# Kernel optimization log

Measured on AMD Instinct MI355X. Metric: run time of the kernel, lower is better.

## Reference

```python
import jax, jax.numpy as jnp
import numpy as np

B, R, C, NH = 8, 64, 256, 8
N = R * R            # 4096 tokens
HD = C // NH         # head dim 32
FF = 3               # focusing factor

def dwconv(x, w, b):
    # x: (B, C, H, W); w: (C, 1, kh, kw) depthwise
    y = jax.lax.conv_general_dilated(
        x, w, window_strides=(1, 1), padding='SAME',
        dimension_numbers=('NCHW', 'OIHW', 'NCHW'),
        feature_group_count=x.shape[1])
    return y + b[None, :, None, None]

def setup_inputs() -> dict:
    key = jax.random.key(0)
    ks = jax.random.split(key, 6)
    return {
        'qkv': jax.random.normal(ks[0], (3, B, N, C), jnp.float32),
        'pos_enc': jax.random.normal(ks[1], (1, N, C), jnp.float32) * 0.02,
        'scale': jax.random.normal(ks[2], (1, 1, C), jnp.float32) * 0.02,
        'w_v': jax.random.normal(ks[3], (C, 1, 3, 3), jnp.float32) * 0.1,
        'b_v': jnp.zeros((C,), jnp.float32),
        'w_dwc': jax.random.normal(ks[4], (HD, 1, 5, 5), jnp.float32) * 0.1,
        'b_dwc': jnp.zeros((HD,), jnp.float32),
    }

def reference(qkv, pos_enc, scale, w_v, b_v, w_dwc, b_dwc):
    q, k, v = qkv[0], qkv[1], qkv[2]          # each (B, N, C)
    # --- LePE: depthwise 3x3 conv on v over full channel dim ---
    v_img = v.transpose(0, 2, 1).reshape(B, C, R, R)
    lepe = dwconv(v_img, w_v, b_v)            # (B, C, R, R)
    lepe = lepe.reshape(B * NH, HD, N).transpose(0, 2, 1)   # (B*h, N, hd)
    v = v_img.reshape(B, C, N).transpose(0, 2, 1)           # (B, N, C)
    # --- focused kernelization ---
    k = k + pos_enc
    sc = jax.nn.softplus(scale)
    q = (jax.nn.relu(q) + 1e-6) / sc
    k = (jax.nn.relu(k) + 1e-6) / sc
    qn = jnp.linalg.norm(q, axis=-1, keepdims=True)
    kn = jnp.linalg.norm(k, axis=-1, keepdims=True)
    q = q ** FF
    k = k ** FF
    q = q / jnp.linalg.norm(q, axis=-1, keepdims=True) * qn
    k = k / jnp.linalg.norm(k, axis=-1, keepdims=True) * kn
    split = lambda x: x.reshape(B, N, NH, HD).transpose(0, 2, 1, 3).reshape(B * NH, N, HD)
    q, k, v = split(q), split(k), split(v)    # (B*h, N, hd)
    # --- linear attention (kv aggregation path: N >> hd) ---
    z = 1.0 / (jnp.einsum('bic,bc->bi', q, k.sum(axis=1)) + 1e-6)
    kv = jnp.einsum('bjc,bjd->bcd', k, v)     # (B*h, hd, hd)
    x = jnp.einsum('bic,bcd,bi->bid', q, kv, z)
    # --- dwc feature mixing on v per head ---
    fm = v.transpose(0, 2, 1).reshape(B * NH, HD, R, R)
    fm = dwconv(fm, w_dwc, b_dwc).reshape(B * NH, HD, N).transpose(0, 2, 1)
    x = x + fm + lepe
    x = x.reshape(B, NH, N, HD).transpose(0, 2, 1, 3).reshape(B, N, C)
    return x
```

## Files before the change

### kernel.cpp

```cpp
#include <hip/hip_runtime.h>
#include <math.h>

#define B_  8
#define R_  64
#define C_  256
#define NH_ 8
#define N_  4096
#define HD_ 32

__device__ __forceinline__ float softplus_rcp(float s) {
    return 1.f / __logf(1.f + __expf(s));
}

__global__ __launch_bounds__(256) void kernelNB2(
        const float* __restrict__ qkv, const float* __restrict__ pos,
        const float* __restrict__ scale,
        float* __restrict__ qs_arr, float* __restrict__ part,
        float* __restrict__ kspart) {
    __shared__ float smem[9472];
    float* kf_s   = smem;
    float* v_s    = smem + 4096;
    float* rsc_s  = smem + 8192;
    float* kred_s = smem + 8448;

    const int t    = threadIdx.x;
    const int wave = t >> 6, lane = t & 63;
    const int c0   = lane * 4;
    const int blk  = blockIdx.x;
    const int tok0 = blk * 32;

    if (t < C_) rsc_s[t] = softplus_rcp(scale[t]);
    __syncthreads();

    const size_t qbase = (size_t)tok0 * C_;
    const size_t kbase = (size_t)B_ * N_ * C_ + qbase;
    const size_t vbase = (size_t)2 * B_ * N_ * C_ + qbase;

    const int h  = t >> 5;
    const int l  = t & 31;
    const int cg = l & 7;
    const int dg = l >> 3;

    const float rs0 = rsc_s[c0 + 0], rs1 = rsc_s[c0 + 1];
    const float rs2 = rsc_s[c0 + 2], rs3 = rsc_s[c0 + 3];

    float acc[4][8];
    #pragma unroll
    for (int ii = 0; ii < 4; ii++)
        #pragma unroll
        for (int jj = 0; jj < 8; jj++) acc[ii][jj] = 0.f;
    float ksp[4] = {0.f, 0.f, 0.f, 0.f};

    for (int tile = 0; tile < 2; tile++) {
        const int nb0 = tile * 16;
        #pragma unroll
        for (int i = 0; i < 4; i++) {
            const int row = wave * 4 + i;
            const int tok = tok0 + nb0 + row;
            const int n   = tok & (N_ - 1);
            const size_t off = (size_t)(nb0 + row) * C_ + c0;
            const float4 q4 = *(const float4*)(qkv + qbase + off);
            const float4 k4 = *(const float4*)(qkv + kbase + off);
            const float4 v4 = *(const float4*)(qkv + vbase + off);
            const float4 p4 = *(const float4*)(pos + (size_t)n * C_ + c0);

            const float qv0 = (fmaxf(q4.x, 0.f) + 1e-6f) * rs0;
            const float qv1 = (fmaxf(q4.y, 0.f) + 1e-6f) * rs1;
            const float qv2 = (fmaxf(q4.z, 0.f) + 1e-6f) * rs2;
            const float qv3 = (fmaxf(q4.w, 0.f) + 1e-6f) * rs3;
            const float kw0 = (fmaxf(k4.x + p4.x, 0.f) + 1e-6f) * rs0;
            const float kw1 = (fmaxf(k4.y + p4.y, 0.f) + 1e-6f) * rs1;
            const float kw2 = (fmaxf(k4.z + p4.z, 0.f) + 1e-6f) * rs2;
            const float kw3 = (fmaxf(k4.w + p4.w, 0.f) + 1e-6f) * rs3;

            const float q30 = qv0 * qv0 * qv0, q31 = qv1 * qv1 * qv1;
            const float q32 = qv2 * qv2 * qv2, q33 = qv3 * qv3 * qv3;
            const float k30 = kw0 * kw0 * kw0, k31 = kw1 * kw1 * kw1;
            const float k32 = kw2 * kw2 * kw2, k33 = kw3 * kw3 * kw3;

            float sq2 = qv0 * qv0 + qv1 * qv1 + qv2 * qv2 + qv3 * qv3;
            float sq6 = q30 * q30 + q31 * q31 + q32 * q32 + q33 * q33;
            float sk2 = kw0 * kw0 + kw1 * kw1 + kw2 * kw2 + kw3 * kw3;
            float sk6 = k30 * k30 + k31 * k31 + k32 * k32 + k33 * k33;
            #pragma unroll
            for (int m = 1; m < 64; m <<= 1) {
                sq2 += __shfl_xor(sq2, m, 64);
                sq6 += __shfl_xor(sq6, m, 64);
                sk2 += __shfl_xor(sk2, m, 64);
                sk6 += __shfl_xor(sk6, m, 64);
            }
            if (lane == 0) qs_arr[tok] = sqrtf(sq2) * rsqrtf(sq6);
            const float ks = sqrtf(sk2) * rsqrtf(sk6);

            float4 kf;
            kf.x = k30 * ks;  kf.y = k31 * ks;
            kf.z = k32 * ks;  kf.w = k33 * ks;
            *(float4*)&kf_s[row * C_ + c0] = kf;
            *(float4*)&v_s [row * C_ + c0] = v4;
            ksp[0] += kf.x;  ksp[1] += kf.y;
            ksp[2] += kf.z;  ksp[3] += kf.w;
        }
        __syncthreads();
        {
            const float* kfp = kf_s + h * HD_ + cg * 4;
            const float* vp  = v_s  + h * HD_ + dg * 8;
            #pragma unroll 4
            for (int nl = 0; nl < 16; nl++) {
                const float4 kr = *(const float4*)(kfp + nl * C_);
                const float4 va = *(const float4*)(vp  + nl * C_);
                const float4 vb = *(const float4*)(vp  + nl * C_ + 4);
                const float kk[4] = {kr.x, kr.y, kr.z, kr.w};
                const float vv[8] = {va.x, va.y, va.z, va.w,
                                     vb.x, vb.y, vb.z, vb.w};
                #pragma unroll
                for (int ii = 0; ii < 4; ii++)
                    #pragma unroll
                    for (int jj = 0; jj < 8; jj++)
                        acc[ii][jj] = fmaf(kk[ii], vv[jj], acc[ii][jj]);
            }
        }
        __syncthreads();
    }

    #pragma unroll
    for (int ii = 0; ii < 4; ii++) {
        float4 a = make_float4(acc[ii][0], acc[ii][1], acc[ii][2], acc[ii][3]);
        float4 b = make_float4(acc[ii][4], acc[ii][5], acc[ii][6], acc[ii][7]);
        const int base = h * 1024 + (cg * 4 + ii) * 32 + dg * 8;
        *(float4*)&smem[base]     = a;
        *(float4*)&smem[base + 4] = b;
    }
    *(float4*)&kred_s[wave * 256 + c0] =
        make_float4(ksp[0], ksp[1], ksp[2], ksp[3]);
    __syncthreads();
    float* pdst = part + (size_t)blk * 8192;
    #pragma unroll
    for (int i = 0; i < 8; i++)
        *(float4*)&pdst[i * 1024 + t * 4] = *(const float4*)&smem[i * 1024 + t * 4];
    kspart[(size_t)blk * 256 + t] =
        kred_s[t] + kred_s[256 + t] + kred_s[512 + t] + kred_s[768 + t];
}

__global__ __launch_bounds__(256) void kernelR(
        const float* __restrict__ part, const float* __restrict__ kspart,
        float* __restrict__ kv_ws, float* __restrict__ ksum_ws) {
    const int t  = threadIdx.x;
    const int bh = blockIdx.x >> 2, q = blockIdx.x & 3;
    const int b  = bh >> 3, h = bh & 7;

    const float* p = part + (size_t)(b * 128) * 8192 + h * 1024 + q * 256 + t;
    float s = 0.f;
    #pragma unroll 4
    for (int j = 0; j < 128; j++) s += p[(size_t)j * 8192];
    kv_ws[bh * 1024 + q * 256 + t] = s;

    if (q == 0 && t < 32) {
        const float* kp = kspart + (size_t)(b * 128) * 256 + h * 32 + t;
        float s2 = 0.f;
        #pragma unroll 8
        for (int j = 0; j < 128; j++) s2 += kp[(size_t)j * 256];
        ksum_ws[bh * 32 + t] = s2;
    }
}

__global__ __launch_bounds__(256) void kernelCD2(
        const float* __restrict__ qkv, const float* __restrict__ qs_arr,
        const float* __restrict__ kv_ws, const float* __restrict__ ksum_ws,
        const float* __restrict__ scale,
        const float* __restrict__ w_v,  const float* __restrict__ b_v,
        const float* __restrict__ w_dwc, const float* __restrict__ b_dwc,
        float* __restrict__ out) {
    __shared__ float v_s[20 * 20 * 32];
    __shared__ float kv_s[1024];
    __shared__ float ks_s[32];
    __shared__ float rsc_s[32];
    const int t    = threadIdx.x;
    const int tile = blockIdx.x;
    const int h    = blockIdx.y;
    const int b    = blockIdx.z;
    const int ty0  = (tile >> 2) * 16, tx0 = (tile & 3) * 16;
    const int bh   = b * NH_ + h;

    ((float4*)kv_s)[t] = ((const float4*)(kv_ws + (size_t)bh * 1024))[t];
    if (t < 32) {
        ks_s[t]  = ksum_ws[bh * HD_ + t];
        rsc_s[t] = softplus_rcp(scale[h * HD_ + t]);
    }

    const float* vb = qkv + (size_t)2 * B_ * N_ * C_ + (size_t)b * N_ * C_ + h * HD_;
    #pragma unroll
    for (int i = 0; i < 13; i++) {
        const int idx = i * 256 + t;
        if (idx < 3200) {
            const int pix = idx >> 3, d4 = (idx & 7) * 4;
            const int yy = pix / 20, xx = pix - yy * 20;
            const int gy = ty0 + yy - 2, gx = tx0 + xx - 2;
            float4 val = make_float4(0.f, 0.f, 0.f, 0.f);
            if (gy >= 0 && gy < R_ && gx >= 0 && gx < R_)
                val = *(const float4*)(vb + (size_t)(gy * R_ + gx) * C_ + d4);
            *(float4*)&v_s[pix * 32 + d4] = val;
        }
    }

    const int c  = t & 31, pg = t >> 5;
    float wv[9], wd[25];
    {
        const float* wvp = w_v + (size_t)(h * HD_ + c) * 9;
        const float* wdp = w_dwc + (size_t)c * 25;
        #pragma unroll
        for (int i = 0; i < 9; i++)  wv[i] = wvp[i];
        #pragma unroll
        for (int i = 0; i < 25; i++) wd[i] = wdp[i];
    }
    const float bias = b_v[h * HD_ + c] + b_dwc[c];
    __syncthreads();

    float res[32];
    #pragma unroll
    for (int r2 = 0; r2 < 2; r2++) {
        const int ty = pg * 2 + r2;
        float win[5][5];
        #pragma unroll
        for (int j = 0; j < 5; j++)
            #pragma unroll
            for (int i = 0; i < 5; i++)
                win[j][i] = v_s[((ty + i) * 20 + j) * 32 + c];
        #pragma unroll
        for (int tx = 0; tx < 16; tx++) {
            float a = bias;
            #pragma unroll
            for (int j = 0; j < 5; j++) {
                const int slot = (tx + j) % 5;
                #pragma unroll
                for (int i = 0; i < 5; i++)
                    a = fmaf(wd[i * 5 + j], win[slot][i], a);
            }
            #pragma unroll
            for (int j = 1; j < 4; j++) {
                const int slot = (tx + j) % 5;
                #pragma unroll
                for (int i = 1; i < 4; i++)
                    a = fmaf(wv[(i - 1) * 3 + (j - 1)], win[slot][i], a);
            }
            res[r2 * 16 + tx] = a;
            if (tx < 15) {
                const int slot = tx % 5;
                #pragma unroll
                for (int i = 0; i < 5; i++)
                    win[slot][i] = v_s[((ty + i) * 20 + (tx + 5)) * 32 + c];
            }
        }
    }
    __syncthreads();
    #pragma unroll
    for (int r2 = 0; r2 < 2; r2++)
        #pragma unroll
        for (int tx = 0; tx < 16; tx++)
            v_s[((pg * 2 + r2) * 16 + tx) * 33 + c] = res[r2 * 16 + tx];
    __syncthreads();

    {
        const int tyy = t >> 4, txx = t & 15;
        const int n   = (ty0 + tyy) * R_ + (tx0 + txx);
        const int tok = b * N_ + n;
        float q[32];
        const float4* qsrc = (const float4*)(qkv + (size_t)tok * C_ + h * HD_);
        #pragma unroll
        for (int i = 0; i < 8; i++) ((float4*)q)[i] = qsrc[i];
        const float qs = qs_arr[tok];
        #pragma unroll
        for (int i = 0; i < 32; i++) {
            const float r = (fmaxf(q[i], 0.f) + 1e-6f) * rsc_s[i];
            q[i] = r * r * r * qs;
        }

        float denom = 1e-6f;
        #pragma unroll
        for (int cc = 0; cc < 32; cc++) denom = fmaf(q[cc], ks_s[cc], denom);
        const float z = 1.f / denom;

        float o[32];
        #pragma unroll
        for (int i = 0; i < 32; i++) o[i] = 0.f;
        #pragma unroll
        for (int cc = 0; cc < 32; cc++) {
            const float qc = q[cc];
            #pragma unroll
            for (int d = 0; d < 32; d++)
                o[d] = fmaf(qc, kv_s[cc * 32 + d], o[d]);
        }
        float4* dst = (float4*)(out + (size_t)tok * C_ + h * HD_);
        #pragma unroll
        for (int i = 0; i < 8; i++) {
            float4 v4;
            v4.x = fmaf(o[i*4+0], z, v_s[t * 33 + i*4+0]);
            v4.y = fmaf(o[i*4+1], z, v_s[t * 33 + i*4+1]);
            v4.z = fmaf(o[i*4+2], z, v_s[t * 33 + i*4+2]);
            v4.w = fmaf(o[i*4+3], z, v_s[t * 33 + i*4+3]);
            dst[i] = v4;
        }
    }
}

extern "C" void kernel_launch(void* const* d_in, const int* in_sizes, int n_in,
                              void* d_out, int out_size, void* d_ws, size_t ws_size,
                              hipStream_t stream) {
    const float* qkv   = (const float*)d_in[0];
    const float* pos   = (const float*)d_in[1];
    const float* scale = (const float*)d_in[2];
    const float* w_v   = (const float*)d_in[3];
    const float* b_v   = (const float*)d_in[4];
    const float* w_dwc = (const float*)d_in[5];
    const float* b_dwc = (const float*)d_in[6];
    float* out = (float*)d_out;

    float* qs_arr  = (float*)d_ws;
    float* part    = qs_arr + (size_t)B_ * N_;
    float* kspart  = part + (size_t)1024 * 8192;
    float* kv_ws   = kspart + (size_t)1024 * 256;
    float* ksum_ws = kv_ws + 64 * 1024;

    kernelNB2<<<dim3(1024), 256, 0, stream>>>(qkv, pos, scale, qs_arr, part, kspart);
    kernelR<<<dim3(256), 256, 0, stream>>>(part, kspart, kv_ws, ksum_ws);
    kernelCD2<<<dim3(16, NH_, B_), 256, 0, stream>>>(qkv, qs_arr, kv_ws, ksum_ws,
                                                     scale, w_v, b_v, w_dwc, b_dwc, out);
}
```

Baseline: 230.6 us.

## Assign 16 lanes per token row in kv-partial kernel with padded LDS rows

The first kernel now has each wave handle 4 token rows at once, 16 lanes per row, each lane covering 16 channels. Row norms then need only a 4-step shuffle reduction instead of 6, and the per-row loop over 4 rows goes away. The shared-memory row stride is padded to 260 floats to reduce bank conflicts. The k column sum is accumulated during the outer-product loop and written straight to global memory, which removes the separate LDS reduction stage. This costs more registers per lane, and the global loads become less contiguous per row.

```diff
diff --git a/kernel.cpp b/kernel.cpp
--- a/kernel.cpp
+++ b/kernel.cpp
@@ -7,43 +7,40 @@
 #define NH_ 8
 #define N_  4096
 #define HD_ 32
+#define LDP 260
 
 __device__ __forceinline__ float softplus_rcp(float s) {
     return 1.f / __logf(1.f + __expf(s));
 }
 
-__global__ __launch_bounds__(256) void kernelNB2(
+__global__ __launch_bounds__(256) void kernelNB3(
         const float* __restrict__ qkv, const float* __restrict__ pos,
         const float* __restrict__ scale,
         float* __restrict__ qs_arr, float* __restrict__ part,
         float* __restrict__ kspart) {
-    __shared__ float smem[9472];
-    float* kf_s   = smem;
-    float* v_s    = smem + 4096;
-    float* rsc_s  = smem + 8192;
-    float* kred_s = smem + 8448;
+    __shared__ float smem[8576];
+    float* kf_s  = smem;
+    float* v_s   = smem + 4160;
+    float* rsc_s = smem + 8320;
 
     const int t    = threadIdx.x;
     const int wave = t >> 6, lane = t & 63;
-    const int c0   = lane * 4;
+    const int tk   = lane >> 4;
+    const int lr   = lane & 15;
     const int blk  = blockIdx.x;
     const int tok0 = blk * 32;
 
-    if (t < C_) rsc_s[t] = softplus_rcp(scale[t]);
-    __syncthreads();
+    rsc_s[t] = softplus_rcp(scale[t]);
 
     const size_t qbase = (size_t)tok0 * C_;
-    const size_t kbase = (size_t)B_ * N_ * C_ + qbase;
-    const size_t vbase = (size_t)2 * B_ * N_ * C_ + qbase;
+    const size_t koff  = (size_t)B_ * N_ * C_;
+    const size_t voff  = (size_t)2 * B_ * N_ * C_;
 
     const int h  = t >> 5;
     const int l  = t & 31;
     const int cg = l & 7;
     const int dg = l >> 3;
 
-    const float rs0 = rsc_s[c0 + 0], rs1 = rsc_s[c0 + 1];
-    const float rs2 = rsc_s[c0 + 2], rs3 = rsc_s[c0 + 3];
-
     float acc[4][8];
     #pragma unroll
     for (int ii = 0; ii < 4; ii++)
@@ -51,54 +48,58 @@
         for (int jj = 0; jj < 8; jj++) acc[ii][jj] = 0.f;
     float ksp[4] = {0.f, 0.f, 0.f, 0.f};
 
+    __syncthreads();
+    float rs[16];
+    #pragma unroll
+    for (int j = 0; j < 4; j++)
+        *(float4*)&rs[j * 4] = *(const float4*)&rsc_s[j * 64 + lr * 4];
+
+    #pragma unroll
     for (int tile = 0; tile < 2; tile++) {
-        const int nb0 = tile * 16;
-        #pragma unroll
-        for (int i = 0; i < 4; i++) {
-            const int row = wave * 4 + i;
-            const int tok = tok0 + nb0 + row;
-            const int n   = tok & (N_ - 1);
-            const size_t off = (size_t)(nb0 + row) * C_ + c0;
-            const float4 q4 = *(const float4*)(qkv + qbase + off);
-            const float4 k4 = *(const float4*)(qkv + kbase + off);
-            const float4 v4 = *(const float4*)(qkv + vbase + off);
-            const float4 p4 = *(const float4*)(pos + (size_t)n * C_ + c0);
-
-            const float qv0 = (fmaxf(q4.x, 0.f) + 1e-6f) * rs0;
-            const float qv1 = (fmaxf(q4.y, 0.f) + 1e-6f) * rs1;
-            const float qv2 = (fmaxf(q4.z, 0.f) + 1e-6f) * rs2;
-            const float qv3 = (fmaxf(q4.w, 0.f) + 1e-6f) * rs3;
-            const float kw0 = (fmaxf(k4.x + p4.x, 0.f) + 1e-6f) * rs0;
-            const float kw1 = (fmaxf(k4.y + p4.y, 0.f) + 1e-6f) * rs1;
-            const float kw2 = (fmaxf(k4.z + p4.z, 0.f) + 1e-6f) * rs2;
-            const float kw3 = (fmaxf(k4.w + p4.w, 0.f) + 1e-6f) * rs3;
-
-            const float q30 = qv0 * qv0 * qv0, q31 = qv1 * qv1 * qv1;
-            const float q32 = qv2 * qv2 * qv2, q33 = qv3 * qv3 * qv3;
-            const float k30 = kw0 * kw0 * kw0, k31 = kw1 * kw1 * kw1;
-            const float k32 = kw2 * kw2 * kw2, k33 = kw3 * kw3 * kw3;
-
-            float sq2 = qv0 * qv0 + qv1 * qv1 + qv2 * qv2 + qv3 * qv3;
-            float sq6 = q30 * q30 + q31 * q31 + q32 * q32 + q33 * q33;
-            float sk2 = kw0 * kw0 + kw1 * kw1 + kw2 * kw2 + kw3 * kw3;
-            float sk6 = k30 * k30 + k31 * k31 + k32 * k32 + k33 * k33;
-            #pragma unroll
-            for (int m = 1; m < 64; m <<= 1) {
-                sq2 += __shfl_xor(sq2, m, 64);
-                sq6 += __shfl_xor(sq6, m, 64);
-                sk2 += __shfl_xor(sk2, m, 64);
-                sk6 += __shfl_xor(sk6, m, 64);
-            }
-            if (lane == 0) qs_arr[tok] = sqrtf(sq2) * rsqrtf(sq6);
-            const float ks = sqrtf(sk2) * rsqrtf(sk6);
-
-            float4 kf;
-            kf.x = k30 * ks;  kf.y = k31 * ks;
-            kf.z = k32 * ks;  kf.w = k33 * ks;
-            *(float4*)&kf_s[row * C_ + c0] = kf;
-            *(float4*)&v_s [row * C_ + c0] = v4;
-            ksp[0] += kf.x;  ksp[1] += kf.y;
-            ksp[2] += kf.z;  ksp[3] += kf.w;
+        const int row  = wave * 4 + tk;
+        const int nrow = tile * 16 + row;
+        const int tok  = tok0 + nrow;
+        const size_t off  = qbase + (size_t)nrow * C_;
+        const size_t poff = (size_t)(tok & (N_ - 1)) * C_;
+
+        float kc[16];
+        float sq2 = 0.f, sq6 = 0.f, sk2 = 0.f, sk6 = 0.f;
+        #pragma unroll
+        for (int j = 0; j < 4; j++) {
+            const int c = j * 64 + lr * 4;
+            const float4 q4 = *(const float4*)(qkv + off + c);
+            const float4 k4 = *(const float4*)(qkv + koff + off + c);
+            const float4 v4 = *(const float4*)(qkv + voff + off + c);
+            const float4 p4 = *(const float4*)(pos + poff + c);
+            *(float4*)&v_s[row * LDP + c] = v4;
+            const float qa[4] = {q4.x, q4.y, q4.z, q4.w};
+            const float ka[4] = {k4.x, k4.y, k4.z, k4.w};
+            const float pa[4] = {p4.x, p4.y, p4.z, p4.w};
+            #pragma unroll
+            for (int e = 0; e < 4; e++) {
+                const float r  = rs[j * 4 + e];
+                const float qv = (fmaxf(qa[e], 0.f) + 1e-6f) * r;
+                const float kw = (fmaxf(ka[e] + pa[e], 0.f) + 1e-6f) * r;
+                sq2 += qv * qv;  sk2 += kw * kw;
+                const float q3 = qv * qv * qv, k3 = kw * kw * kw;
+                sq6 += q3 * q3;  sk6 += k3 * k3;
+                kc[j * 4 + e] = k3;
+            }
+        }
+        #pragma unroll
+        for (int m = 1; m < 16; m <<= 1) {
+            sq2 += __shfl_xor(sq2, m, 64);
+            sq6 += __shfl_xor(sq6, m, 64);
+            sk2 += __shfl_xor(sk2, m, 64);
+            sk6 += __shfl_xor(sk6, m, 64);
+        }
+        if (lr == 0) qs_arr[tok] = sqrtf(sq2) * rsqrtf(sq6);
+        const float ks = sqrtf(sk2) * rsqrtf(sk6);
+        #pragma unroll
+        for (int j = 0; j < 4; j++) {
+            const float4 kf4 = make_float4(kc[j*4+0] * ks, kc[j*4+1] * ks,
+                                           kc[j*4+2] * ks, kc[j*4+3] * ks);
+            *(float4*)&kf_s[row * LDP + j * 64 + lr * 4] = kf4;
         }
         __syncthreads();
         {
@@ -106,9 +107,11 @@
             const float* vp  = v_s  + h * HD_ + dg * 8;
             #pragma unroll 4
             for (int nl = 0; nl < 16; nl++) {
-                const float4 kr = *(const float4*)(kfp + nl * C_);
-                const float4 va = *(const float4*)(vp  + nl * C_);
-                const float4 vb = *(const float4*)(vp  + nl * C_ + 4);
+                const float4 kr = *(const float4*)(kfp + nl * LDP);
+                const float4 va = *(const float4*)(vp  + nl * LDP);
+                const float4 vb = *(const float4*)(vp  + nl * LDP + 4);
+                ksp[0] += kr.x;  ksp[1] += kr.y;
+                ksp[2] += kr.z;  ksp[3] += kr.w;
                 const float kk[4] = {kr.x, kr.y, kr.z, kr.w};
                 const float vv[8] = {va.x, va.y, va.z, va.w,
                                      vb.x, vb.y, vb.z, vb.w};
@@ -124,21 +127,20 @@
 
     #pragma unroll
     for (int ii = 0; ii < 4; ii++) {
-        float4 a = make_float4(acc[ii][0], acc[ii][1], acc[ii][2], acc[ii][3]);
-        float4 b = make_float4(acc[ii][4], acc[ii][5], acc[ii][6], acc[ii][7]);
+        const float4 a = make_float4(acc[ii][0], acc[ii][1], acc[ii][2], acc[ii][3]);
+        const float4 b = make_float4(acc[ii][4], acc[ii][5], acc[ii][6], acc[ii][7]);
         const int base = h * 1024 + (cg * 4 + ii) * 32 + dg * 8;
         *(float4*)&smem[base]     = a;
         *(float4*)&smem[base + 4] = b;
     }
-    *(float4*)&kred_s[wave * 256 + c0] =
-        make_float4(ksp[0], ksp[1], ksp[2], ksp[3]);
+    if (dg == 0)
+        *(float4*)&kspart[(size_t)blk * 256 + h * 32 + cg * 4] =
+            make_float4(ksp[0], ksp[1], ksp[2], ksp[3]);
     __syncthreads();
     float* pdst = part + (size_t)blk * 8192;
     #pragma unroll
     for (int i = 0; i < 8; i++)
         *(float4*)&pdst[i * 1024 + t * 4] = *(const float4*)&smem[i * 1024 + t * 4];
-    kspart[(size_t)blk * 256 + t] =
-        kred_s[t] + kred_s[256 + t] + kred_s[512 + t] + kred_s[768 + t];
 }
 
 __global__ __launch_bounds__(256) void kernelR(
@@ -320,7 +322,7 @@
     float* kv_ws   = kspart + (size_t)1024 * 256;
     float* ksum_ws = kv_ws + 64 * 1024;
 
-    kernelNB2<<<dim3(1024), 256, 0, stream>>>(qkv, pos, scale, qs_arr, part, kspart);
+    kernelNB3<<<dim3(1024), 256, 0, stream>>>(qkv, pos, scale, qs_arr, part, kspart);
     kernelR<<<dim3(256), 256, 0, stream>>>(part, kspart, kv_ws, ksum_ws);
     kernelCD2<<<dim3(16, NH_, B_), 256, 0, stream>>>(qkv, qs_arr, kv_ws, ksum_ws,
                                                      scale, w_v, b_v, w_dwc, b_dwc, out);
```

Result: no change. 228.9 us (-0.7%).
